# Kernel optimization log

Measured on AMD Instinct MI355X. Metric: run time of the kernel, lower is better.

The kernel has to match this reference:

```python
import jax, jax.numpy as jnp
import numpy as np

B, S, D, H = 4, 2048, 1024, 16
DK = D // H

def setup_inputs() -> dict:
    key = jax.random.key(0)
    ks = jax.random.split(key, 11)
    sc = 1.0 / np.sqrt(D)
    return {
        "query": jax.random.normal(ks[0], (B, S, D), jnp.float32),
        "key": jax.random.normal(ks[1], (B, S, D), jnp.float32),
        "value": jax.random.normal(ks[2], (B, S, D), jnp.float32),
        "Wq": jax.random.normal(ks[3], (D, D), jnp.float32) * sc,
        "bq": jnp.zeros((D,), jnp.float32),
        "Wk": jax.random.normal(ks[4], (D, D), jnp.float32) * sc,
        "bk": jnp.zeros((D,), jnp.float32),
        "Wv": jax.random.normal(ks[5], (D, D), jnp.float32) * sc,
        "bv": jnp.zeros((D,), jnp.float32),
        "Wo": jax.random.normal(ks[6], (D, D), jnp.float32) * sc,
        "bo": jnp.zeros((D,), jnp.float32),
    }

def _mha(query, key, value, Wq, bq, Wk, bk, Wv, bv, Wo, bo):
    # in_linear{0,1,2}: y = x @ W.T + b  (MetaLinearLayer, weight [out,in])
    def proj(x, W, b):
        y = jnp.einsum('bsd,ed->bse', x, W) + b
        return y.reshape(B, S, H, DK).transpose(0, 2, 1, 3)  # [B,H,S,DK]
    q = proj(query, Wq, bq)
    k = proj(key, Wk, bk)
    v = proj(value, Wv, bv)
    # scores = QK^T / sqrt(d_k)  -> [B,H,S,S] (materialized as in original)
    scores = jnp.einsum('bhqd,bhkd->bhqk', q, k) / jnp.sqrt(jnp.float32(DK))
    p_attn = jax.nn.softmax(scores, axis=-1)
    # dropout is identity in eval/reference mode
    x = jnp.einsum('bhqk,bhkd->bhqd', p_attn, v)
    x = x.transpose(0, 2, 1, 3).reshape(B, S, D)
    return jnp.einsum('bsd,ed->bse', x, Wo) + bo

def reference(query, key, value, Wq, bq, Wk, bk, Wv, bv, Wo, bo):
    return _mha(query, key, value, Wq, bq, Wk, bk, Wv, bv, Wo, bo)
```

## Files before the change

kernel.cpp:

```cpp
#include <hip/hip_runtime.h>
#include <stdint.h>

typedef __attribute__((ext_vector_type(4))) float f32x4;
typedef __attribute__((ext_vector_type(8))) __bf16 bf16x8;
typedef __attribute__((ext_vector_type(8))) unsigned short u16x8;
typedef __attribute__((ext_vector_type(4))) uint32_t u32x4;

#define GLOBAL_AS __attribute__((address_space(1)))
#define LDS_AS    __attribute__((address_space(3)))

__device__ __forceinline__ void lds_load16(const void* g, void* l) {
  __builtin_amdgcn_global_load_lds((const GLOBAL_AS uint32_t*)(uintptr_t)g,
                                   (LDS_AS uint32_t*)(uintptr_t)l, 16, 0, 0);
}

__device__ __forceinline__ unsigned short f2bf(float f) {
  uint32_t u = __builtin_bit_cast(uint32_t, f);
  u += 0x7fffu + ((u >> 16) & 1u);
  return (unsigned short)(u >> 16);
}

__device__ __forceinline__ uint32_t pk_bf16(float a, float b) {
#if __has_builtin(__builtin_amdgcn_cvt_pk_bf16_f32)
  return __builtin_bit_cast(uint32_t, __builtin_amdgcn_cvt_pk_bf16_f32(a, b));
#else
  return (uint32_t)f2bf(a) | ((uint32_t)f2bf(b) << 16);
#endif
}

__device__ __forceinline__ float exp2f_fast(float x) {
#if __has_builtin(__builtin_amdgcn_exp2f)
  return __builtin_amdgcn_exp2f(x);
#else
  return __expf(x * 0.6931471805599453f);
#endif
}

__device__ __forceinline__ bf16x8 pack8(const f32x4 a, const f32x4 b) {
  u32x4 d;
  d.x = pk_bf16(a[0], a[1]);
  d.y = pk_bf16(a[2], a[3]);
  d.z = pk_bf16(b[0], b[1]);
  d.w = pk_bf16(b[2], b[3]);
  return __builtin_bit_cast(bf16x8, d);
}

#define QK_SCALE 0.18033688011112042f

__global__ void cast_all(const float* __restrict__ q, const float* __restrict__ k,
                         const float* __restrict__ v, const float* __restrict__ Wq,
                         const float* __restrict__ Wk, const float* __restrict__ Wv,
                         const float* __restrict__ Wo, unsigned short* __restrict__ dst) {
  const int bid = blockIdx.x;
  const float* src;
  int rel;
  if (bid < 24576) {
    const int seg = bid >> 13;
    rel = bid & 8191;
    src = (seg == 0) ? q : (seg == 1) ? k : v;
  } else {
    const int w = (bid - 24576) >> 10;
    rel = (bid - 24576) & 1023;
    src = (w == 0) ? Wq : (w == 1) ? Wk : (w == 2) ? Wv : Wo;
  }
  const size_t di = (size_t)bid * 1024 + threadIdx.x * 4;
  const size_t si = (size_t)rel * 1024 + threadIdx.x * 4;
  const float4 val = *(const float4*)(src + si);
  ushort4 o;
  o.x = f2bf(val.x); o.y = f2bf(val.y); o.z = f2bf(val.z); o.w = f2bf(val.w);
  *(ushort4*)(dst + di) = o;
}

__global__ __launch_bounds__(256, 2)
void gemm_qkv(const unsigned short* __restrict__ xq, const unsigned short* __restrict__ xk,
              const unsigned short* __restrict__ xv, const unsigned short* __restrict__ wq,
              const unsigned short* __restrict__ wk, const unsigned short* __restrict__ wv,
              const float* __restrict__ bq, const float* __restrict__ bk,
              const float* __restrict__ bv,
              unsigned short* __restrict__ Qh, unsigned short* __restrict__ Kh,
              unsigned short* __restrict__ Vt)
{
  __shared__ __align__(16) unsigned short As[128 * 32];
  __shared__ __align__(16) unsigned short Bs[128 * 32];

  const int gy = blockIdx.y, gx = blockIdx.x;
  const unsigned short* A  = (gy == 0) ? xq : (gy == 1) ? xk : wv;
  const unsigned short* Bw = (gy == 0) ? wq : (gy == 1) ? wk : xv;
  const float* bias        = (gy == 0) ? bq : (gy == 1) ? bk : bv;

  int m0, n0, N;
  if (gy < 2) { m0 = (gx >> 3) * 128; n0 = (gx & 7) * 128; N = 1024; }
  else        { m0 = (gx & 7) * 128;  n0 = (gx >> 3) * 128; N = 8192; }
  const int K = 1024;

  const int tid  = threadIdx.x;
  const int wave = tid >> 6;
  const int lane = tid & 63;
  const int wm = wave >> 1, wn = wave & 1;
  const int quad = lane >> 4, l15 = lane & 15;

  f32x4 acc[4][4];
#pragma unroll
  for (int i = 0; i < 4; ++i)
#pragma unroll
    for (int j = 0; j < 4; ++j) acc[i][j] = f32x4{0.f, 0.f, 0.f, 0.f};

  const int sr = lane >> 2;
  const int sc = (lane & 3) * 8;
  const unsigned short* Ag0 = A  + (size_t)(m0 + wave * 16 + sr) * K + sc;
  const unsigned short* Ag1 = Ag0 + (size_t)64 * K;
  const unsigned short* Bg0 = Bw + (size_t)(n0 + wave * 16 + sr) * K + sc;
  const unsigned short* Bg1 = Bg0 + (size_t)64 * K;
  unsigned short* AsW0 = &As[wave * 512];
  unsigned short* AsW1 = &As[2048 + wave * 512];
  unsigned short* BsW0 = &Bs[wave * 512];
  unsigned short* BsW1 = &Bs[2048 + wave * 512];

  for (int k0 = 0; k0 < K; k0 += 32) {
    lds_load16(Ag0 + k0, AsW0);
    lds_load16(Ag1 + k0, AsW1);
    lds_load16(Bg0 + k0, BsW0);
    lds_load16(Bg1 + k0, BsW1);
    __syncthreads();

    bf16x8 af[4], bfr[4];
#pragma unroll
    for (int i = 0; i < 4; ++i)
      af[i] = *(const bf16x8*)&As[(wm * 64 + i * 16 + l15) * 32 + quad * 8];
#pragma unroll
    for (int j = 0; j < 4; ++j)
      bfr[j] = *(const bf16x8*)&Bs[(wn * 64 + j * 16 + l15) * 32 + quad * 8];
#pragma unroll
    for (int i = 0; i < 4; ++i)
#pragma unroll
      for (int j = 0; j < 4; ++j)
        acc[i][j] = __builtin_amdgcn_mfma_f32_16x16x32_bf16(af[i], bfr[j], acc[i][j], 0, 0, 0);
    __syncthreads();
  }

  if (gy < 2) {
    unsigned short* out = (gy == 0) ? Qh : Kh;
    const float scl = (gy == 0) ? QK_SCALE : 1.0f;
    float bj[4];
#pragma unroll
    for (int j = 0; j < 4; ++j) bj[j] = bias[n0 + wn * 64 + j * 16 + l15];
#pragma unroll
    for (int i = 0; i < 4; ++i) {
      const int mbase = m0 + wm * 64 + i * 16 + quad * 4;
#pragma unroll
      for (int j = 0; j < 4; ++j) {
        const int n = n0 + wn * 64 + j * 16 + l15;
#pragma unroll
        for (int r = 0; r < 4; ++r) {
          const int m = mbase + r;
          const float vv = (acc[i][j][r] + bj[j]) * scl;
          const size_t idx = ((((size_t)(m >> 11) * 16 + (n >> 6)) << 11) + (size_t)(m & 2047)) * 64 + (n & 63);
          out[idx] = f2bf(vv);
        }
      }
    }
  } else {
#pragma unroll
    for (int i = 0; i < 4; ++i) {
      const int mbase = m0 + wm * 64 + i * 16 + quad * 4;
      float bm[4];
#pragma unroll
      for (int r = 0; r < 4; ++r) bm[r] = bias[mbase + r];
#pragma unroll
      for (int j = 0; j < 4; ++j) {
        const int n = n0 + wn * 64 + j * 16 + l15;
#pragma unroll
        for (int r = 0; r < 4; ++r)
          Vt[(size_t)(mbase + r) * N + n] = f2bf(acc[i][j][r] + bm[r]);
      }
    }
  }
}

__global__ __launch_bounds__(256, 2)
void flash_attn(const unsigned short* __restrict__ Qh,
                const unsigned short* __restrict__ Kh,
                const unsigned short* __restrict__ VtG,
                unsigned short* __restrict__ Xo)
{
  __shared__ __align__(16) unsigned short Ks[128 * 72];
  __shared__ __align__(16) unsigned short Vs[64 * 136];

  const int qb = blockIdx.x, h = blockIdx.y, b = blockIdx.z;
  const int tid = threadIdx.x, wave = tid >> 6, lane = tid & 63;
  const int quad = lane >> 4, l15 = lane & 15;

  const size_t bh = (((size_t)b * 16 + h) << 17);
  const unsigned short* Qg = Qh + bh + ((size_t)qb << 13);
  const unsigned short* Kg = Kh + bh;
  const unsigned short* Vg = VtG + ((size_t)(h * 64)) * 8192 + (size_t)b * 2048;

#pragma unroll
  for (int p = 0; p < 4; ++p) {
    const int c = tid + p * 256;
    u16x8 qv = *(const u16x8*)(Qg + c * 8);
    *(u16x8*)&Ks[(c >> 3) * 72 + (c & 7) * 8] = qv;
  }
  __syncthreads();
  bf16x8 aq[2][2];
#pragma unroll
  for (int i = 0; i < 2; ++i)
#pragma unroll
    for (int d = 0; d < 2; ++d)
      aq[i][d] = *(const bf16x8*)&Ks[(wave * 32 + i * 16 + l15) * 72 + d * 32 + quad * 8];

  f32x4 oacc[2][4];
  f32x4 lacc[2];
#pragma unroll
  for (int i = 0; i < 2; ++i) {
#pragma unroll
    for (int jd = 0; jd < 4; ++jd) oacc[i][jd] = f32x4{0.f, 0.f, 0.f, 0.f};
    lacc[i] = f32x4{0.f, 0.f, 0.f, 0.f};
  }

  const uint32_t one2 = 0x3F803F80u;
  const u32x4 onesU{one2, one2, one2, one2};
  const bf16x8 onesB = __builtin_bit_cast(bf16x8, onesU);

  const int rb = (l15 >> 3) * 16 + ((l15 >> 2) & 1) * 4 + (l15 & 3);

  u16x8 kreg[4], vreg[4];
#pragma unroll
  for (int p = 0; p < 4; ++p) {
    const int c = tid + p * 256;
    kreg[p] = *(const u16x8*)(Kg + c * 8);
    vreg[p] = *(const u16x8*)(Vg + (size_t)(c >> 4) * 8192 + (c & 15) * 8);
  }

  for (int kb = 0; kb < 16; ++kb) {
    __syncthreads();
#pragma unroll
    for (int p = 0; p < 4; ++p) {
      const int c = tid + p * 256;
      const int kr = c >> 3;
      const int krp = (kr & ~12) | ((kr & 4) << 1) | ((kr & 8) >> 1);
      *(u16x8*)&Ks[krp * 72 + (c & 7) * 8] = kreg[p];
      *(u16x8*)&Vs[(c >> 4) * 136 + (c & 15) * 8] = vreg[p];
    }
    __syncthreads();

#pragma unroll 1
    for (int hh = 0; hh < 2; ++hh) {
      f32x4 s[2][4];
#pragma unroll
      for (int i = 0; i < 2; ++i)
#pragma unroll
        for (int j = 0; j < 4; ++j) s[i][j] = f32x4{0.f, 0.f, 0.f, 0.f};
#pragma unroll
      for (int d = 0; d < 2; ++d)
#pragma unroll
        for (int j = 0; j < 4; ++j) {
          const int kk = j >> 1, p2 = j & 1;
          bf16x8 kf = *(const bf16x8*)&Ks[(hh * 64 + kk * 32 + p2 * 8 + rb) * 72 + d * 32 + quad * 8];
#pragma unroll
          for (int i = 0; i < 2; ++i)
            s[i][j] = __builtin_amdgcn_mfma_f32_16x16x32_bf16(kf, aq[i][d], s[i][j], 0, 0, 0);
        }

#pragma unroll
      for (int i = 0; i < 2; ++i)
#pragma unroll
        for (int j = 0; j < 4; ++j)
#pragma unroll
          for (int r = 0; r < 4; ++r)
            s[i][j][r] = exp2f_fast(s[i][j][r]);

      bf16x8 ap[2][2];
#pragma unroll
      for (int i = 0; i < 2; ++i)
#pragma unroll
        for (int kk = 0; kk < 2; ++kk)
          ap[i][kk] = pack8(s[i][2 * kk], s[i][2 * kk + 1]);

#pragma unroll
      for (int i = 0; i < 2; ++i)
#pragma unroll
        for (int kk = 0; kk < 2; ++kk)
          lacc[i] = __builtin_amdgcn_mfma_f32_16x16x32_bf16(ap[i][kk], onesB, lacc[i], 0, 0, 0);

      if (kb < 15) {
        if (hh == 0) {
          const size_t ko = ((size_t)(kb + 1) << 13);
#pragma unroll
          for (int p = 0; p < 4; ++p) {
            const int c = tid + p * 256;
            kreg[p] = *(const u16x8*)(Kg + ko + c * 8);
          }
        } else {
#pragma unroll
          for (int p = 0; p < 4; ++p) {
            const int c = tid + p * 256;
            vreg[p] = *(const u16x8*)(Vg + (size_t)(c >> 4) * 8192 + (kb + 1) * 128 + (c & 15) * 8);
          }
        }
      }

#pragma unroll
      for (int kk = 0; kk < 2; ++kk) {
#pragma unroll
        for (int jd = 0; jd < 4; ++jd) {
          bf16x8 bv = *(const bf16x8*)&Vs[(jd * 16 + l15) * 136 + (hh * 2 + kk) * 32 + quad * 8];
#pragma unroll
          for (int i = 0; i < 2; ++i)
            oacc[i][jd] = __builtin_amdgcn_mfma_f32_16x16x32_bf16(ap[i][kk], bv, oacc[i][jd], 0, 0, 0);
        }
      }
    }
  }

#pragma unroll
  for (int i = 0; i < 2; ++i)
#pragma unroll
    for (int r = 0; r < 4; ++r) {
      const float inv = 1.f / lacc[i][r];
      const int srow = qb * 128 + wave * 32 + i * 16 + quad * 4 + r;
      const size_t obase = (((size_t)b << 11) + srow) * 1024 + (h << 6);
#pragma unroll
      for (int jd = 0; jd < 4; ++jd)
        Xo[obase + jd * 16 + l15] = f2bf(oacc[i][jd][r] * inv);
    }
}

__global__ __launch_bounds__(256, 2)
void gemm_out(const unsigned short* __restrict__ A,
              const unsigned short* __restrict__ Bw,
              const float* __restrict__ bias,
              float* __restrict__ Cout)
{
  __shared__ __align__(16) unsigned short As[128 * 32];
  __shared__ __align__(16) unsigned short Bs[128 * 32];

  const int tid  = threadIdx.x;
  const int wave = tid >> 6;
  const int lane = tid & 63;
  const int wm = wave >> 1, wn = wave & 1;
  const int quad = lane >> 4, l15 = lane & 15;
  const int m0 = blockIdx.y * 128;
  const int n0 = blockIdx.x * 128;
  const int K = 1024, N = 1024;

  f32x4 acc[4][4];
#pragma unroll
  for (int i = 0; i < 4; ++i)
#pragma unroll
    for (int j = 0; j < 4; ++j) acc[i][j] = f32x4{0.f, 0.f, 0.f, 0.f};

  const int sr = lane >> 2;
  const int sc = (lane & 3) * 8;
  const unsigned short* Ag0 = A  + (size_t)(m0 + wave * 16 + sr) * K + sc;
  const unsigned short* Ag1 = Ag0 + (size_t)64 * K;
  const unsigned short* Bg0 = Bw + (size_t)(n0 + wave * 16 + sr) * K + sc;
  const unsigned short* Bg1 = Bg0 + (size_t)64 * K;
  unsigned short* AsW0 = &As[wave * 512];
  unsigned short* AsW1 = &As[2048 + wave * 512];
  unsigned short* BsW0 = &Bs[wave * 512];
  unsigned short* BsW1 = &Bs[2048 + wave * 512];

  for (int k0 = 0; k0 < K; k0 += 32) {
    lds_load16(Ag0 + k0, AsW0);
    lds_load16(Ag1 + k0, AsW1);
    lds_load16(Bg0 + k0, BsW0);
    lds_load16(Bg1 + k0, BsW1);
    __syncthreads();

    bf16x8 af[4], bfr[4];
#pragma unroll
    for (int i = 0; i < 4; ++i)
      af[i] = *(const bf16x8*)&As[(wm * 64 + i * 16 + l15) * 32 + quad * 8];
#pragma unroll
    for (int j = 0; j < 4; ++j)
      bfr[j] = *(const bf16x8*)&Bs[(wn * 64 + j * 16 + l15) * 32 + quad * 8];
#pragma unroll
    for (int i = 0; i < 4; ++i)
#pragma unroll
      for (int j = 0; j < 4; ++j)
        acc[i][j] = __builtin_amdgcn_mfma_f32_16x16x32_bf16(af[i], bfr[j], acc[i][j], 0, 0, 0);
    __syncthreads();
  }

  float bj[4];
#pragma unroll
  for (int j = 0; j < 4; ++j) bj[j] = bias[n0 + wn * 64 + j * 16 + l15];

#pragma unroll
  for (int i = 0; i < 4; ++i) {
    const int mbase = m0 + wm * 64 + i * 16 + quad * 4;
#pragma unroll
    for (int j = 0; j < 4; ++j) {
      const int n = n0 + wn * 64 + j * 16 + l15;
#pragma unroll
      for (int r = 0; r < 4; ++r)
        Cout[(size_t)(mbase + r) * N + n] = acc[i][j][r] + bj[j];
    }
  }
}

extern "C" void kernel_launch(void* const* d_in, const int* in_sizes, int n_in,
                              void* d_out, int out_size, void* d_ws, size_t ws_size,
                              hipStream_t stream) {
  const float* q  = (const float*)d_in[0];
  const float* k  = (const float*)d_in[1];
  const float* v  = (const float*)d_in[2];
  const float* Wq = (const float*)d_in[3];
  const float* bq = (const float*)d_in[4];
  const float* Wk = (const float*)d_in[5];
  const float* bk = (const float*)d_in[6];
  const float* Wv = (const float*)d_in[7];
  const float* bv = (const float*)d_in[8];
  const float* Wo = (const float*)d_in[9];
  const float* bo = (const float*)d_in[10];

  const int B = 4, S = 2048, D = 1024, H = 16;
  const size_t NX = (size_t)B * S * D;
  const size_t NW = (size_t)D * D;

  unsigned short* xq = (unsigned short*)d_ws;
  unsigned short* xk = xq + NX;
  unsigned short* xv = xk + NX;
  unsigned short* wq = xv + NX;
  unsigned short* wk = wq + NW;
  unsigned short* wv = wk + NW;
  unsigned short* wo = wv + NW;
  unsigned short* Qh = wo + NW;
  unsigned short* Kh = Qh + NX;
  unsigned short* Vt = Kh + NX;
  unsigned short* xo = Vt + NX;

  cast_all<<<28672, 256, 0, stream>>>(q, k, v, Wq, Wk, Wv, Wo, xq);
  gemm_qkv<<<dim3(512, 3), 256, 0, stream>>>(xq, xk, xv, wq, wk, wv, bq, bk, bv, Qh, Kh, Vt);
  flash_attn<<<dim3(S / 128, H, B), 256, 0, stream>>>(Qh, Kh, Vt, xo);
  gemm_out<<<dim3(D / 128, (B * S) / 128), 256, 0, stream>>>(xo, wo, bo, (float*)d_out);
}
```

Baseline: 370.1 us.

## Deepen GEMM K-tile with XOR-swizzled LDS, remap attention blocks, add MFMA priorities

Both GEMM kernels now stage a 64-wide K slice per iteration instead of 32. The LDS layout is XOR-swizzled, which cuts barrier count per K and avoids bank conflicts on the fragment reads. The flash attention kernel remaps its flat block index so that consecutive blocks spread across heads and batches, likely for better cache/XCD locality. It also wraps the MFMA sections in s_setprio raises and moves the row-sum MFMA after the prefetch loads. LDS use per GEMM block doubles, which could affect occupancy.

```diff
diff --git a/kernel.cpp b/kernel.cpp
--- a/kernel.cpp
+++ b/kernel.cpp
@@ -80,8 +80,8 @@
               unsigned short* __restrict__ Qh, unsigned short* __restrict__ Kh,
               unsigned short* __restrict__ Vt)
 {
-  __shared__ __align__(16) unsigned short As[128 * 32];
-  __shared__ __align__(16) unsigned short Bs[128 * 32];
+  __shared__ __align__(16) unsigned short As[128 * 64];
+  __shared__ __align__(16) unsigned short Bs[128 * 64];
 
   const int gy = blockIdx.y, gx = blockIdx.x;
   const unsigned short* A  = (gy == 0) ? xq : (gy == 1) ? xk : wv;
@@ -105,36 +105,40 @@
 #pragma unroll
     for (int j = 0; j < 4; ++j) acc[i][j] = f32x4{0.f, 0.f, 0.f, 0.f};
 
-  const int sr = lane >> 2;
-  const int sc = (lane & 3) * 8;
-  const unsigned short* Ag0 = A  + (size_t)(m0 + wave * 16 + sr) * K + sc;
-  const unsigned short* Ag1 = Ag0 + (size_t)64 * K;
-  const unsigned short* Bg0 = Bw + (size_t)(n0 + wave * 16 + sr) * K + sc;
-  const unsigned short* Bg1 = Bg0 + (size_t)64 * K;
-  unsigned short* AsW0 = &As[wave * 512];
-  unsigned short* AsW1 = &As[2048 + wave * 512];
-  unsigned short* BsW0 = &Bs[wave * 512];
-  unsigned short* BsW1 = &Bs[2048 + wave * 512];
-
-  for (int k0 = 0; k0 < K; k0 += 32) {
-    lds_load16(Ag0 + k0, AsW0);
-    lds_load16(Ag1 + k0, AsW1);
-    lds_load16(Bg0 + k0, BsW0);
-    lds_load16(Bg1 + k0, BsW1);
-    __syncthreads();
-
-    bf16x8 af[4], bfr[4];
-#pragma unroll
-    for (int i = 0; i < 4; ++i)
-      af[i] = *(const bf16x8*)&As[(wm * 64 + i * 16 + l15) * 32 + quad * 8];
-#pragma unroll
-    for (int j = 0; j < 4; ++j)
-      bfr[j] = *(const bf16x8*)&Bs[(wn * 64 + j * 16 + l15) * 32 + quad * 8];
-#pragma unroll
-    for (int i = 0; i < 4; ++i)
+  const int sr8 = lane >> 3;
+  const int scx = ((lane & 7) ^ (sr8 & 7)) * 8;
+  const unsigned short* Agb = A  + (size_t)(m0 + wave * 8 + sr8) * K + scx;
+  const unsigned short* Bgb = Bw + (size_t)(n0 + wave * 8 + sr8) * K + scx;
+  unsigned short* AsW = &As[wave * 8 * 64];
+  unsigned short* BsW = &Bs[wave * 8 * 64];
+
+  const int colx0 = (quad * 8) ^ ((l15 & 7) * 8);
+  const int colx1 = (32 + quad * 8) ^ ((l15 & 7) * 8);
+
+  for (int k0 = 0; k0 < K; k0 += 64) {
+#pragma unroll
+    for (int t = 0; t < 4; ++t) {
+      lds_load16(Agb + (size_t)(t * 32) * K + k0, AsW + t * 32 * 64);
+      lds_load16(Bgb + (size_t)(t * 32) * K + k0, BsW + t * 32 * 64);
+    }
+    __syncthreads();
+
+#pragma unroll
+    for (int kd = 0; kd < 2; ++kd) {
+      const int colx = kd ? colx1 : colx0;
+      bf16x8 af[4], bfr[4];
+#pragma unroll
+      for (int i = 0; i < 4; ++i)
+        af[i] = *(const bf16x8*)&As[(wm * 64 + i * 16 + l15) * 64 + colx];
 #pragma unroll
       for (int j = 0; j < 4; ++j)
-        acc[i][j] = __builtin_amdgcn_mfma_f32_16x16x32_bf16(af[i], bfr[j], acc[i][j], 0, 0, 0);
+        bfr[j] = *(const bf16x8*)&Bs[(wn * 64 + j * 16 + l15) * 64 + colx];
+#pragma unroll
+      for (int i = 0; i < 4; ++i)
+#pragma unroll
+        for (int j = 0; j < 4; ++j)
+          acc[i][j] = __builtin_amdgcn_mfma_f32_16x16x32_bf16(af[i], bfr[j], acc[i][j], 0, 0, 0);
+    }
     __syncthreads();
   }
 
@@ -186,7 +190,10 @@
   __shared__ __align__(16) unsigned short Ks[128 * 72];
   __shared__ __align__(16) unsigned short Vs[64 * 136];
 
-  const int qb = blockIdx.x, h = blockIdx.y, b = blockIdx.z;
+  const int fid = blockIdx.x + (blockIdx.y << 4) + (blockIdx.z << 8);
+  const int wid = ((fid & 7) << 7) + (fid >> 3);
+  const int qb = wid & 15, h = (wid >> 4) & 15, b = wid >> 8;
+
   const int tid = threadIdx.x, wave = tid >> 6, lane = tid & 63;
   const int quad = lane >> 4, l15 = lane & 15;
 
@@ -251,6 +258,7 @@
       for (int i = 0; i < 2; ++i)
 #pragma unroll
         for (int j = 0; j < 4; ++j) s[i][j] = f32x4{0.f, 0.f, 0.f, 0.f};
+      __builtin_amdgcn_s_setprio(1);
 #pragma unroll
       for (int d = 0; d < 2; ++d)
 #pragma unroll
@@ -261,6 +269,7 @@
           for (int i = 0; i < 2; ++i)
             s[i][j] = __builtin_amdgcn_mfma_f32_16x16x32_bf16(kf, aq[i][d], s[i][j], 0, 0, 0);
         }
+      __builtin_amdgcn_s_setprio(0);
 
 #pragma unroll
       for (int i = 0; i < 2; ++i)
@@ -276,12 +285,6 @@
 #pragma unroll
         for (int kk = 0; kk < 2; ++kk)
           ap[i][kk] = pack8(s[i][2 * kk], s[i][2 * kk + 1]);
-
-#pragma unroll
-      for (int i = 0; i < 2; ++i)
-#pragma unroll
-        for (int kk = 0; kk < 2; ++kk)
-          lacc[i] = __builtin_amdgcn_mfma_f32_16x16x32_bf16(ap[i][kk], onesB, lacc[i], 0, 0, 0);
 
       if (kb < 15) {
         if (hh == 0) {
@@ -300,6 +303,12 @@
         }
       }
 
+      __builtin_amdgcn_s_setprio(1);
+#pragma unroll
+      for (int i = 0; i < 2; ++i)
+#pragma unroll
+        for (int kk = 0; kk < 2; ++kk)
+          lacc[i] = __builtin_amdgcn_mfma_f32_16x16x32_bf16(ap[i][kk], onesB, lacc[i], 0, 0, 0);
 #pragma unroll
       for (int kk = 0; kk < 2; ++kk) {
 #pragma unroll
@@ -310,6 +319,7 @@
             oacc[i][jd] = __builtin_amdgcn_mfma_f32_16x16x32_bf16(ap[i][kk], bv, oacc[i][jd], 0, 0, 0);
         }
       }
+      __builtin_amdgcn_s_setprio(0);
     }
   }
 
@@ -332,8 +342,8 @@
               const float* __restrict__ bias,
               float* __restrict__ Cout)
 {
-  __shared__ __align__(16) unsigned short As[128 * 32];
-  __shared__ __align__(16) unsigned short Bs[128 * 32];
+  __shared__ __align__(16) unsigned short As[128 * 64];
+  __shared__ __align__(16) unsigned short Bs[128 * 64];
 
   const int tid  = threadIdx.x;
   const int wave = tid >> 6;
@@ -350,36 +360,40 @@
 #pragma unroll
     for (int j = 0; j < 4; ++j) acc[i][j] = f32x4{0.f, 0.f, 0.f, 0.f};
 
-  const int sr = lane >> 2;
-  const int sc = (lane & 3) * 8;
-  const unsigned short* Ag0 = A  + (size_t)(m0 + wave * 16 + sr) * K + sc;
-  const unsigned short* Ag1 = Ag0 + (size_t)64 * K;
-  const unsigned short* Bg0 = Bw + (size_t)(n0 + wave * 16 + sr) * K + sc;
-  const unsigned short* Bg1 = Bg0 + (size_t)64 * K;
-  unsigned short* AsW0 = &As[wave * 512];
-  unsigned short* AsW1 = &As[2048 + wave * 512];
-  unsigned short* BsW0 = &Bs[wave * 512];
-  unsigned short* BsW1 = &Bs[2048 + wave * 512];
-
-  for (int k0 = 0; k0 < K; k0 += 32) {
-    lds_load16(Ag0 + k0, AsW0);
-    lds_load16(Ag1 + k0, AsW1);
-    lds_load16(Bg0 + k0, BsW0);
-    lds_load16(Bg1 + k0, BsW1);
-    __syncthreads();
-
-    bf16x8 af[4], bfr[4];
-#pragma unroll
-    for (int i = 0; i < 4; ++i)
-      af[i] = *(const bf16x8*)&As[(wm * 64 + i * 16 + l15) * 32 + quad * 8];
-#pragma unroll
-    for (int j = 0; j < 4; ++j)
-      bfr[j] = *(const bf16x8*)&Bs[(wn * 64 + j * 16 + l15) * 32 + quad * 8];
-#pragma unroll
-    for (int i = 0; i < 4; ++i)
+  const int sr8 = lane >> 3;
+  const int scx = ((lane & 7) ^ (sr8 & 7)) * 8;
+  const unsigned short* Agb = A  + (size_t)(m0 + wave * 8 + sr8) * K + scx;
+  const unsigned short* Bgb = Bw + (size_t)(n0 + wave * 8 + sr8) * K + scx;
+  unsigned short* AsW = &As[wave * 8 * 64];
+  unsigned short* BsW = &Bs[wave * 8 * 64];
+
+  const int colx0 = (quad * 8) ^ ((l15 & 7) * 8);
+  const int colx1 = (32 + quad * 8) ^ ((l15 & 7) * 8);
+
+  for (int k0 = 0; k0 < K; k0 += 64) {
+#pragma unroll
+    for (int t = 0; t < 4; ++t) {
+      lds_load16(Agb + (size_t)(t * 32) * K + k0, AsW + t * 32 * 64);
+      lds_load16(Bgb + (size_t)(t * 32) * K + k0, BsW + t * 32 * 64);
+    }
+    __syncthreads();
+
+#pragma unroll
+    for (int kd = 0; kd < 2; ++kd) {
+      const int colx = kd ? colx1 : colx0;
+      bf16x8 af[4], bfr[4];
+#pragma unroll
+      for (int i = 0; i < 4; ++i)
+        af[i] = *(const bf16x8*)&As[(wm * 64 + i * 16 + l15) * 64 + colx];
 #pragma unroll
       for (int j = 0; j < 4; ++j)
-        acc[i][j] = __builtin_amdgcn_mfma_f32_16x16x32_bf16(af[i], bfr[j], acc[i][j], 0, 0, 0);
+        bfr[j] = *(const bf16x8*)&Bs[(wn * 64 + j * 16 + l15) * 64 + colx];
+#pragma unroll
+      for (int i = 0; i < 4; ++i)
+#pragma unroll
+        for (int j = 0; j < 4; ++j)
+          acc[i][j] = __builtin_amdgcn_mfma_f32_16x16x32_bf16(af[i], bfr[j], acc[i][j], 0, 0, 0);
+    }
     __syncthreads();
   }
 
```

Measured after the change: 344.2 us. -7.0%, faster.
